# Kernel optimization log

Measured on AMD Instinct MI355X. Metric: run time of the kernel, lower is better.

## Reference

```python
import jax, jax.numpy as jnp
import numpy as np

D = 1024
H = 16
DH = D // H
L = 128  # max_pos_len
B = 4
T = 1024
SCALE = float(np.sqrt(D / H))


def setup_inputs() -> dict:
    key = jax.random.key(0)
    ks = jax.random.split(key, 9)
    x_q = jax.random.normal(ks[0], (B, T, D), dtype=jnp.float32)
    x_k = jax.random.normal(ks[1], (B, T, D), dtype=jnp.float32)
    x_v = jax.random.normal(ks[2], (B, T, D), dtype=jnp.float32)
    mask = jax.random.randint(ks[3], (B, 1, 1, T), 0, 2) == 1  # bool, True = masked
    Wq = jax.random.normal(ks[4], (D, D), dtype=jnp.float32) * 0.02
    Wk = jax.random.normal(ks[5], (D, D), dtype=jnp.float32) * 0.02
    Wv = jax.random.normal(ks[6], (D, D), dtype=jnp.float32) * 0.02
    Wo = jax.random.normal(ks[7], (D, D), dtype=jnp.float32) * 0.02
    pos_emb = jax.random.normal(ks[8], (2 * L + 1, DH), dtype=jnp.float32)
    return {"x_q": x_q, "x_k": x_k, "x_v": x_v, "mask": mask,
            "Wq": Wq, "Wk": Wk, "Wv": Wv, "Wo": Wo, "pos_emb": pos_emb}


def reference(x_q, x_k, x_v, mask, Wq, Wk, Wv, Wo, pos_emb):
    # nn.Linear(bias=False): y = x @ W.T
    def split_heads(x):  # (B,T,D) -> (B,H,T,DH)
        return x.reshape(B, -1, H, DH).transpose(0, 2, 1, 3)

    Q = split_heads(x_q @ Wq.T)
    K = split_heads(x_k @ Wk.T)
    V = split_heads(x_v @ Wv.T)

    logits = jnp.einsum('bhqd,bhkd->bhqk', Q, K)

    # arrange_char_pos_embedding: indices[q,k] = clamp(k-q, -L, L) + L
    rel = jnp.clip(jnp.arange(T)[None, :] - jnp.arange(T)[:, None], -L, L) + L
    arranged_pos = pos_emb[rel]  # (T_Q, T_K, DH)
    pos_logits = jnp.einsum('bhqd,qkd->bhqk', Q, arranged_pos)

    logits = (logits + pos_logits) / SCALE
    logits = jnp.where(mask, -jnp.inf, logits)  # mask broadcasts (B,1,1,T)
    attn = jax.nn.softmax(logits, axis=-1)  # dropout p=0.0 -> identity

    combined = jnp.einsum('bhqk,bhkd->bhqd', attn, V)
    heads_concat = combined.transpose(0, 2, 1, 3).reshape(B, -1, D)
    return heads_concat @ Wo.T
```

## Files before the change

kernel.cpp:

```cpp
#include <hip/hip_runtime.h>
#include <hip/hip_bf16.h>
#include <stdint.h>

typedef __attribute__((ext_vector_type(8))) short short8;
typedef __attribute__((ext_vector_type(4))) float f32x4;

__device__ __forceinline__ uint16_t f2bf(float f) {
    union { float f; uint32_t u; } v; v.f = f;
    uint32_t r = v.u + 0x7FFF + ((v.u >> 16) & 1);
    return (uint16_t)(r >> 16);
}
__device__ __forceinline__ float bf2f(uint16_t u) {
    union { uint32_t u; float f; } v; v.u = ((uint32_t)u) << 16;
    return v.f;
}
__device__ __forceinline__ float exp2_raw(float x) {
    float r;
    asm("v_exp_f32 %0, %1" : "=v"(r) : "v"(x));
    return r;
}
__device__ __forceinline__ uint32_t cvt_pk_bf16(float lo, float hi) {
    uint32_t r;
    asm("v_cvt_pk_bf16_f32 %0, %1, %2" : "=v"(r) : "v"(lo), "v"(hi));
    return r;
}

template<int F32>
__device__ __forceinline__ uint4 load8(const void* p, size_t off) {
    if (F32) {
        const float* f = (const float*)p + off;
        float4 f0 = *(const float4*)f;
        float4 f1 = *(const float4*)(f + 4);
        uint4 r;
        r.x = (uint32_t)f2bf(f0.x) | ((uint32_t)f2bf(f0.y) << 16);
        r.y = (uint32_t)f2bf(f0.z) | ((uint32_t)f2bf(f0.w) << 16);
        r.z = (uint32_t)f2bf(f1.x) | ((uint32_t)f2bf(f1.y) << 16);
        r.w = (uint32_t)f2bf(f1.z) | ((uint32_t)f2bf(f1.w) << 16);
        return r;
    } else {
        return *(const uint4*)((const uint16_t*)p + off);
    }
}

#define GLDS(gp, lp) __builtin_amdgcn_global_load_lds( \
    (const __attribute__((address_space(1))) void*)(gp), \
    (__attribute__((address_space(3))) void*)(lp), 16, 0, 0)

struct CvtSeg { const float* s; uint16_t* d; int n8; };
struct CvtArgs {
    CvtSeg seg[9]; int nseg;
    const void* mraw; unsigned long long* mbits; uint16_t* mvals;
};

__global__ __launch_bounds__(256) void cvt_bf16(CvtArgs a)
{
    if (blockIdx.x == 0) {
        __shared__ int flags[3];
        __shared__ uint8_t mloc[4096];
        const uint32_t* w = (const uint32_t*)a.mraw;
        const uint8_t* b8 = (const uint8_t*)a.mraw;
        const int t = threadIdx.x;
        if (t < 3) flags[t] = 0;
        __syncthreads();
        int fbyte = 0, ff32 = 0, fodd = 0;
        for (int i = t; i < 1024; i += 256) {
            uint32_t v = w[i];
            if (v != 0u && v != 1u && v != 0x3F800000u) fbyte = 1;
            if (v == 0x3F800000u) ff32 = 1;
            if ((i & 1) && v != 0u) fodd = 1;
        }
        if (fbyte) atomicOr(&flags[0], 1);
        if (ff32)  atomicOr(&flags[1], 1);
        if (fodd)  atomicOr(&flags[2], 1);
        __syncthreads();
        int mode;
        if (flags[0]) mode = 1;
        else if (flags[1]) mode = 0;
        else if (!flags[2]) mode = 2;
        else mode = 0;
        for (int k = t; k < 4096; k += 256) {
            int val;
            if (mode == 1)      val = (b8[k] != 0);
            else if (mode == 2) val = (w[2 * k] != 0u);
            else                val = (w[k] != 0u);
            mloc[k] = (uint8_t)val;
        }
        __syncthreads();
        for (int k = t; k < 4096; k += 256)
            a.mvals[k] = mloc[k] ? (uint16_t)0 : (uint16_t)0x3F80;
        if (t < 64) {
            uint64_t bits = 0;
#pragma unroll
            for (int i = 0; i < 64; ++i)
                bits |= (uint64_t)mloc[t * 64 + i] << i;
            a.mbits[t] = bits;
        }
    }
    const int tid = blockIdx.x * 256 + threadIdx.x;
    const int stride = gridDim.x * 256;
    for (int s = 0; s < a.nseg; ++s) {
        const float* src = a.seg[s].s;
        uint16_t* dst = a.seg[s].d;
        const int n8 = a.seg[s].n8;
        if (src) {
            for (int i = tid; i < n8; i += stride)
                *(uint4*)(dst + (size_t)i * 8) = load8<1>(src, (size_t)i * 8);
        } else {
            const uint4 z = {0u, 0u, 0u, 0u};
            for (int i = tid; i < n8; i += stride)
                *(uint4*)(dst + (size_t)i * 8) = z;
        }
    }
}

__global__ __launch_bounds__(256) void gemm128_qkv(
    const uint16_t* __restrict__ xq, const uint16_t* __restrict__ xk, const uint16_t* __restrict__ xv,
    const uint16_t* __restrict__ Wq, const uint16_t* __restrict__ Wk, const uint16_t* __restrict__ Wv,
    uint16_t* __restrict__ Qh, uint16_t* __restrict__ Khd, uint16_t* __restrict__ Vt,
    const unsigned long long* __restrict__ mbits)
{
    __shared__ alignas(16) uint16_t As[2][128 * 32];
    __shared__ alignas(16) uint16_t Bs[2][128 * 32];

    const int z = blockIdx.z;
    const uint16_t* A = (z == 0) ? xq : (z == 1) ? xk : xv;
    const uint16_t* B = (z == 0) ? Wq : (z == 1) ? Wk : Wv;
    uint16_t* C = (z == 0) ? Qh : (z == 1) ? Khd : Vt;
    const int cm = (z == 2) ? 2 : 1;
    const int bm = blockIdx.x, bn = blockIdx.y;
    const int K = 1024;

    const int t = threadIdx.x;
    const int lane = t & 63, wave = t >> 6;
    const int lrow = lane & 15, quad = lane >> 4;
    const int wr = (wave >> 1) * 64, wc = (wave & 1) * 64;
    const int g_row = wave * 16 + (lane >> 2);
    const int g_col = (lane & 3) * 8;

    const f32x4 fz = {0.f, 0.f, 0.f, 0.f};
    f32x4 acc[4][4];
#pragma unroll
    for (int i = 0; i < 4; ++i)
#pragma unroll
        for (int j = 0; j < 4; ++j) acc[i][j] = fz;

    for (int k0 = 0; k0 < K; k0 += 64) {
        __syncthreads();
#pragma unroll
        for (int kh = 0; kh < 2; ++kh) {
            const int kk = k0 + kh * 32;
            GLDS(A + (size_t)(bm * 128 + g_row) * K + kk + g_col,      As[kh] + wave * 512);
            GLDS(A + (size_t)(bm * 128 + g_row + 64) * K + kk + g_col, As[kh] + wave * 512 + 2048);
            GLDS(B + (size_t)(bn * 128 + g_row) * K + kk + g_col,      Bs[kh] + wave * 512);
            GLDS(B + (size_t)(bn * 128 + g_row + 64) * K + kk + g_col, Bs[kh] + wave * 512 + 2048);
        }
        __syncthreads();

#pragma unroll
        for (int kh = 0; kh < 2; ++kh) {
            short8 a[4], b[4];
#pragma unroll
            for (int i = 0; i < 4; ++i)
                a[i] = *(const short8*)(As[kh] + (wr + i * 16 + lrow) * 32 + quad * 8);
#pragma unroll
            for (int j = 0; j < 4; ++j)
                b[j] = *(const short8*)(Bs[kh] + (wc + j * 16 + lrow) * 32 + quad * 8);
#pragma unroll
            for (int i = 0; i < 4; ++i)
#pragma unroll
                for (int j = 0; j < 4; ++j)
                    acc[i][j] = __builtin_amdgcn_mfma_f32_16x16x32_bf16(a[i], b[j], acc[i][j], 0, 0, 0);
        }
    }

    if (cm == 2) {
        __syncthreads();
        uint16_t* scr = As[0] + wave * 1024;
        const int mg0 = bm * 128 + wr;
        const int widx = __builtin_amdgcn_readfirstlane((mg0 >> 10) * 16 + ((mg0 & 1023) >> 6));
        const uint64_t mword = mbits[widx];
        const uint64_t mw64 = mword >> ((lane & 1) * 8);
#pragma unroll
        for (int i = 0; i < 4; ++i)
#pragma unroll
            for (int j = 0; j < 4; ++j) {
                uint2 pk;
                pk.x = (uint32_t)f2bf(acc[i][j][0]) | ((uint32_t)f2bf(acc[i][j][1]) << 16);
                pk.y = (uint32_t)f2bf(acc[i][j][2]) | ((uint32_t)f2bf(acc[i][j][3]) << 16);
                *(uint2*)(scr + lrow * 16 + quad * 4) = pk;
                if (lane < 32) {
                    int n = lane >> 1, m8 = (lane & 1) * 8;
                    short8 vv = *(const short8*)(scr + n * 16 + m8);
                    int ng = bn * 128 + wc + j * 16 + n;
                    int hh = ng >> 6, d = ng & 63;
                    int mg = bm * 128 + wr + i * 16;
                    int bb = mg >> 10, tl = (mg & 1023) + m8;
                    uint32_t eb = (uint32_t)(mw64 >> (i * 16)) & 0xFFu;
                    if (eb) {
                        union { short8 s; uint32_t u[4]; } uw;
                        uw.s = vv;
#pragma unroll
                        for (int c = 0; c < 4; ++c) {
                            uint32_t km = (((eb >> (2 * c)) & 1) ? 0u : 0x0000FFFFu)
                                        | (((eb >> (2 * c + 1)) & 1) ? 0u : 0xFFFF0000u);
                            uw.u[c] &= km;
                        }
                        vv = uw.s;
                    }
                    size_t addr = (size_t)(bb * 16 + hh) * 65536
                                + (size_t)((tl >> 6) * 4096
                                           + ((d >> 4) * 2 + ((tl >> 5) & 1)) * 512
                                           + ((tl >> 3) & 3) * 128 + (d & 15) * 8);
                    *(short8*)(C + addr) = vv;
                }
            }
        return;
    }

#pragma unroll
    for (int i = 0; i < 4; ++i)
#pragma unroll
        for (int j = 0; j < 4; ++j)
#pragma unroll
            for (int r = 0; r < 4; ++r) {
                int m = bm * 128 + wr + i * 16 + quad * 4 + r;
                int n = bn * 128 + wc + j * 16 + lrow;
                int bb = m >> 10, tt = m & 1023, hh = n >> 6, d = n & 63;
                C[(((size_t)bb * 16 + hh) * 1024 + tt) * 64 + d] = f2bf(acc[i][j][r]);
            }
}

__global__ __launch_bounds__(256) void gemm_out(
    const uint16_t* __restrict__ A, const uint16_t* __restrict__ B,
    float* __restrict__ C, int M, int N, int K)
{
    __shared__ alignas(16) uint16_t As[2][64 * 32];
    __shared__ alignas(16) uint16_t Bs[2][128 * 32];

    const int t = threadIdx.x;
    const int lane = t & 63, wave = t >> 6;
    const int lrow = lane & 15, quad = lane >> 4;
    const int wr = (wave >> 1) * 32, wc = (wave & 1) * 64;
    const int g_row = wave * 16 + (lane >> 2);
    const int g_col = (lane & 3) * 8;
    const int bm = blockIdx.x, bn = blockIdx.y;

    const f32x4 fz = {0.f, 0.f, 0.f, 0.f};
    f32x4 acc[2][4];
#pragma unroll
    for (int i = 0; i < 2; ++i)
#pragma unroll
        for (int j = 0; j < 4; ++j) acc[i][j] = fz;

    for (int k0 = 0; k0 < K; k0 += 64) {
        __syncthreads();
#pragma unroll
        for (int kh = 0; kh < 2; ++kh) {
            const int kk = k0 + kh * 32;
            GLDS(A + (size_t)(bm * 64 + g_row) * K + kk + g_col,       As[kh] + wave * 512);
            GLDS(B + (size_t)(bn * 128 + g_row) * K + kk + g_col,      Bs[kh] + wave * 512);
            GLDS(B + (size_t)(bn * 128 + g_row + 64) * K + kk + g_col, Bs[kh] + wave * 512 + 2048);
        }
        __syncthreads();

#pragma unroll
        for (int kh = 0; kh < 2; ++kh) {
            short8 a[2], b[4];
#pragma unroll
            for (int i = 0; i < 2; ++i)
                a[i] = *(const short8*)(As[kh] + (wr + i * 16 + lrow) * 32 + quad * 8);
#pragma unroll
            for (int j = 0; j < 4; ++j)
                b[j] = *(const short8*)(Bs[kh] + (wc + j * 16 + lrow) * 32 + quad * 8);
#pragma unroll
            for (int i = 0; i < 2; ++i)
#pragma unroll
                for (int j = 0; j < 4; ++j)
                    acc[i][j] = __builtin_amdgcn_mfma_f32_16x16x32_bf16(a[i], b[j], acc[i][j], 0, 0, 0);
        }
    }

#pragma unroll
    for (int i = 0; i < 2; ++i)
#pragma unroll
        for (int j = 0; j < 4; ++j)
#pragma unroll
            for (int r = 0; r < 4; ++r) {
                int m = bm * 64 + wr + i * 16 + quad * 4 + r;
                int n = bn * 128 + wc + j * 16 + lrow;
                C[(size_t)m * N + n] = acc[i][j][r];
            }
}

#define FA_SM(KB_)                                                              \
{                                                                               \
    const int diff = (KB_) - qb;                                                \
    if (diff <= -192 || diff >= 144) {                                          \
        const bool low = (diff <= -192);                                        \
        _Pragma("unroll")                                                       \
        for (int j = 0; j < 4; ++j) {                                           \
            float e[4];                                                         \
            _Pragma("unroll")                                                   \
            for (int r = 0; r < 4; ++r) {                                       \
                float pc = low ? pcl[r] : pch[r];                               \
                e[r] = exp2_raw(__builtin_fmaf(s[j][r], CS, pc));               \
            }                                                                   \
            const uint32_t p01 = cvt_pk_bf16(e[0], e[1]);                       \
            const uint32_t p23 = cvt_pk_bf16(e[2], e[3]);                       \
            const int col = j * 16 + lrow;                                      \
            const int rw = quad * 4;                                            \
            Pl[wave][rw + 0][col] = (uint16_t)p01;                              \
            Pl[wave][rw + 1][col] = (uint16_t)(p01 >> 16);                      \
            Pl[wave][rw + 2][col] = (uint16_t)p23;                              \
            Pl[wave][rw + 3][col] = (uint16_t)(p23 >> 16);                      \
        }                                                                       \
    } else {                                                                    \
        _Pragma("unroll")                                                       \
        for (int j = 0; j < 4; ++j) {                                           \
            const int key = (KB_) + j * 16 + lrow;                              \
            float e[4];                                                         \
            _Pragma("unroll")                                                   \
            for (int r = 0; r < 4; ++r) {                                       \
                int q = qb + quad * 4 + r;                                      \
                int ql = q & 63;                                                \
                int rel = min(max(key - q, -128), 128) + 128;                   \
                float p = bf2f(Qpos_l[ql][rel]);                                \
                e[r] = exp2_raw(__builtin_fmaf(s[j][r], CS, p));                \
            }                                                                   \
            const uint32_t p01 = cvt_pk_bf16(e[0], e[1]);                       \
            const uint32_t p23 = cvt_pk_bf16(e[2], e[3]);                       \
            const int col = j * 16 + lrow;                                      \
            const int rw = quad * 4;                                            \
            Pl[wave][rw + 0][col] = (uint16_t)p01;                              \
            Pl[wave][rw + 1][col] = (uint16_t)(p01 >> 16);                      \
            Pl[wave][rw + 2][col] = (uint16_t)p23;                              \
            Pl[wave][rw + 3][col] = (uint16_t)(p23 >> 16);                      \
        }                                                                       \
    }                                                                           \
    ap0 = *(const short8*)(&Pl[wave][lrow][quad * 8]);                          \
    ap1 = *(const short8*)(&Pl[wave][lrow][32 + quad * 8]);                     \
}

__global__ __launch_bounds__(256, 3) void flash_attn(
    const uint16_t* __restrict__ Qh, const uint16_t* __restrict__ Kh,
    const uint16_t* __restrict__ Vt, const uint16_t* __restrict__ pos,
    const uint16_t* __restrict__ maskv, uint16_t* __restrict__ comb)
{
    const int blk = blockIdx.x;
    const int jj = blk >> 3;
    const int bh = (blk & 7) * 8 + (jj >> 4);
    const int qt = jj & 15;
    const int b = bh >> 4;
    const int h = bh & 15;
    const int t = threadIdx.x;
    const int lane = t & 63;
    const int wave = t >> 6;
    const int lrow = lane & 15;
    const int quad = lane >> 4;
    const int qb = qt * 64 + wave * 16;
    const int lane8 = lane * 8;

    __shared__ alignas(16) uint16_t Ks[4096];
    __shared__ alignas(16) uint16_t Qpos_l[64][277];
    __shared__ alignas(16) uint16_t Pl[4][16][72];

    const uint16_t* Kp = Kh + (size_t)bh * 65536;
    const uint16_t* Vp = Vt + (size_t)bh * 65536;
    const uint16_t* mkb = maskv + (size_t)b * 1024;

    const int sg_r = lane >> 2;
    const int sg_c = ((lane & 3) ^ ((sg_r >> 1) & 3)) * 8;
    const int hw = wave >> 1;
    const int gw = (wave & 1) * 2;
    const int rdc = (quad ^ ((lrow >> 1) & 3)) * 8;

    const float CS = 0.18033688011f;

#pragma unroll
    for (int gg = 0; gg < 2; ++gg) {
        int g = gw + gg;
        GLDS(Kp + (size_t)(g * 16 + sg_r) * 64 + hw * 32 + sg_c, &Ks[hw * 2048 + g * 512]);
    }

    const uint16_t* Qp = Qh + ((size_t)bh * 1024 + qb) * 64;
    short8 aq0 = *(const short8*)(Qp + (size_t)lrow * 64 + quad * 8);
    short8 aq1 = *(const short8*)(Qp + (size_t)lrow * 64 + 32 + quad * 8);

    const f32x4 fz = {0.f, 0.f, 0.f, 0.f};

#pragma unroll 4
    for (int nt = 0; nt < 17; ++nt) {
        short8 pb0 = *(const short8*)(pos + (size_t)(nt * 16 + lrow) * 64 + quad * 8);
        short8 pb1 = *(const short8*)(pos + (size_t)(nt * 16 + lrow) * 64 + 32 + quad * 8);
        f32x4 c = __builtin_amdgcn_mfma_f32_16x16x32_bf16(aq0, pb0, fz, 0, 0, 0);
        c = __builtin_amdgcn_mfma_f32_16x16x32_bf16(aq1, pb1, c, 0, 0, 0);
        const uint32_t p01 = cvt_pk_bf16(c[0] * CS, c[1] * CS);
        const uint32_t p23 = cvt_pk_bf16(c[2] * CS, c[3] * CS);
        const int row = wave * 16 + quad * 4;
        const int col = nt * 16 + lrow;
        Qpos_l[row + 0][col] = (uint16_t)p01;
        Qpos_l[row + 1][col] = (uint16_t)(p01 >> 16);
        Qpos_l[row + 2][col] = (uint16_t)p23;
        Qpos_l[row + 3][col] = (uint16_t)(p23 >> 16);
    }

    float pcl[4], pch[4];
#pragma unroll
    for (int r = 0; r < 4; ++r) {
        int ql = wave * 16 + quad * 4 + r;
        pcl[r] = bf2f(Qpos_l[ql][0]);
        pch[r] = bf2f(Qpos_l[ql][256]);
    }

    f32x4 o[4] = {fz, fz, fz, fz};
    f32x4 lacc = fz;
    short8 ap0, ap1;

    for (int ti = 0; ti < 16; ++ti) {
        const int kb = ti * 64;
        __syncthreads();
        short8 kr[8];
#pragma unroll
        for (int j = 0; j < 4; ++j) {
            kr[j * 2 + 0] = *(const short8*)(Ks + (j * 16 + lrow) * 32 + rdc);
            kr[j * 2 + 1] = *(const short8*)(Ks + 2048 + (j * 16 + lrow) * 32 + rdc);
        }
        __syncthreads();
        if (ti < 15) {
#pragma unroll
            for (int gg = 0; gg < 2; ++gg) {
                int g = gw + gg;
                GLDS(Kp + (size_t)(kb + 64 + g * 16 + sg_r) * 64 + hw * 32 + sg_c,
                     &Ks[hw * 2048 + g * 512]);
            }
        }
        const uint16_t* vb = Vp + (size_t)ti * 4096;
        short8 vv[8];
#pragma unroll
        for (int sl = 0; sl < 8; ++sl)
            vv[sl] = *(const short8*)(vb + sl * 512 + lane8);
        short8 bm0 = *(const short8*)(mkb + kb + quad * 8);
        short8 bm1 = *(const short8*)(mkb + kb + 32 + quad * 8);

        f32x4 s[4];
        __builtin_amdgcn_s_setprio(1);
#pragma unroll
        for (int j = 0; j < 4; ++j) {
            s[j] = __builtin_amdgcn_mfma_f32_16x16x32_bf16(aq0, kr[j * 2 + 0], fz, 0, 0, 0);
            s[j] = __builtin_amdgcn_mfma_f32_16x16x32_bf16(aq1, kr[j * 2 + 1], s[j], 0, 0, 0);
        }
        __builtin_amdgcn_s_setprio(0);

        FA_SM(kb)

        __builtin_amdgcn_s_setprio(1);
#pragma unroll
        for (int dt = 0; dt < 4; ++dt) {
            o[dt] = __builtin_amdgcn_mfma_f32_16x16x32_bf16(ap0, vv[dt * 2 + 0], o[dt], 0, 0, 0);
            o[dt] = __builtin_amdgcn_mfma_f32_16x16x32_bf16(ap1, vv[dt * 2 + 1], o[dt], 0, 0, 0);
        }
        lacc = __builtin_amdgcn_mfma_f32_16x16x32_bf16(ap0, bm0, lacc, 0, 0, 0);
        lacc = __builtin_amdgcn_mfma_f32_16x16x32_bf16(ap1, bm1, lacc, 0, 0, 0);
        __builtin_amdgcn_s_setprio(0);
    }

    float inv[4];
#pragma unroll
    for (int r = 0; r < 4; ++r) inv[r] = 1.0f / lacc[r];

#pragma unroll
    for (int dt = 0; dt < 4; ++dt)
#pragma unroll
        for (int r = 0; r < 4; ++r) {
            size_t row = (size_t)b * 1024 + qb + quad * 4 + r;
            size_t col = (size_t)h * 64 + dt * 16 + lrow;
            comb[row * 1024 + col] = f2bf(o[dt][r] * inv[r]);
        }
}

extern "C" void kernel_launch(void* const* d_in, const int* in_sizes, int n_in,
                              void* d_out, int out_size, void* d_ws, size_t ws_size,
                              hipStream_t stream)
{
    const float* x_q = (const float*)d_in[0];
    const float* x_k = (const float*)d_in[1];
    const float* x_v = (const float*)d_in[2];
    const void*  msk = d_in[3];
    const float* Wq  = (const float*)d_in[4];
    const float* Wk  = (const float*)d_in[5];
    const float* Wv  = (const float*)d_in[6];
    const float* Wo  = (const float*)d_in[7];
    const float* pos = (const float*)d_in[8];

    char* ws = (char*)d_ws;
    const size_t MB = 1u << 20;
    uint16_t* Qh   = (uint16_t*)(ws);
    uint16_t* Khd  = (uint16_t*)(ws + 8 * MB);
    uint16_t* Vt   = (uint16_t*)(ws + 16 * MB);
    uint16_t* xqb  = (uint16_t*)(ws + 24 * MB);
    uint16_t* xkb  = (uint16_t*)(ws + 32 * MB);
    uint16_t* xvb  = (uint16_t*)(ws + 40 * MB);
    uint16_t* Wqb  = (uint16_t*)(ws + 48 * MB);
    uint16_t* Wkb  = (uint16_t*)(ws + 50 * MB);
    uint16_t* Wvb  = (uint16_t*)(ws + 52 * MB);
    uint16_t* Wob  = (uint16_t*)(ws + 54 * MB);
    uint16_t* posb = (uint16_t*)(ws + 56 * MB);
    unsigned long long* mbits = (unsigned long long*)(ws + 56 * MB + 65536);
    uint16_t* mvals = (uint16_t*)(ws + 56 * MB + 65536 + 4096);
    uint16_t* comb = xqb;

    CvtArgs ca{};
    int ns = 0;
    ca.seg[ns++] = {x_q, xqb, 524288};
    ca.seg[ns++] = {x_k, xkb, 524288};
    ca.seg[ns++] = {x_v, xvb, 524288};
    ca.seg[ns++] = {Wq, Wqb, 131072};
    ca.seg[ns++] = {Wk, Wkb, 131072};
    ca.seg[ns++] = {Wv, Wvb, 131072};
    ca.seg[ns++] = {Wo, Wob, 131072};
    ca.seg[ns++] = {pos, posb, 2056};
    ca.seg[ns++] = {nullptr, posb + 16448, 120};
    ca.nseg = ns;
    ca.mraw = msk;
    ca.mbits = mbits;
    ca.mvals = mvals;
    cvt_bf16<<<dim3(512), dim3(256), 0, stream>>>(ca);

    gemm128_qkv<<<dim3(32, 8, 3), dim3(256), 0, stream>>>(
        xqb, xkb, xvb, Wqb, Wkb, Wvb, Qh, Khd, Vt, mbits);

    flash_attn<<<dim3(1024), dim3(256), 0, stream>>>(Qh, Khd, Vt, posb, mvals, comb);

    gemm_out<<<dim3(64, 8), dim3(256), 0, stream>>>(
        comb, Wob, (float*)d_out, 4096, 1024, 1024);
}
```

Before: 224.1 us.

## Software-pipeline PV MFMA one tile behind QK and softmax in flash attention

Restructures the key-tile loop so the P·V and row-sum MFMAs for tile ti-1 are issued alongside the QK MFMAs for tile ti, with a peeled prologue and epilogue. V and mask loads for a tile are issued after its softmax and consumed one iteration later, giving the global loads more time to land. The intent is to overlap MFMA work with the exp/softmax VALU phase and hide V load latency. In exchange, the V registers stay live across iterations, which raises register pressure under the 3-blocks-per-CU launch bound.

Measured after the change: 230.4 us. 1.03x slower.

```diff
diff --git a/kernel.cpp b/kernel.cpp
--- a/kernel.cpp
+++ b/kernel.cpp
@@ -341,6 +341,27 @@
     ap1 = *(const short8*)(&Pl[wave][lrow][32 + quad * 8]);                     \
 }
 
+#define FA_LOADV(TI_)                                                           \
+{                                                                               \
+    const uint16_t* vb = Vp + (size_t)(TI_) * 4096;                             \
+    _Pragma("unroll")                                                           \
+    for (int sl = 0; sl < 8; ++sl)                                              \
+        vv[sl] = *(const short8*)(vb + sl * 512 + lane8);                       \
+    bmc0 = *(const short8*)(mkb + (TI_) * 64 + quad * 8);                       \
+    bmc1 = *(const short8*)(mkb + (TI_) * 64 + 32 + quad * 8);                  \
+}
+
+#define FA_PV                                                                   \
+{                                                                               \
+    _Pragma("unroll")                                                           \
+    for (int dt = 0; dt < 4; ++dt) {                                            \
+        o[dt] = __builtin_amdgcn_mfma_f32_16x16x32_bf16(ap0, vv[dt * 2 + 0], o[dt], 0, 0, 0); \
+        o[dt] = __builtin_amdgcn_mfma_f32_16x16x32_bf16(ap1, vv[dt * 2 + 1], o[dt], 0, 0, 0); \
+    }                                                                           \
+    lacc = __builtin_amdgcn_mfma_f32_16x16x32_bf16(ap0, bmc0, lacc, 0, 0, 0);   \
+    lacc = __builtin_amdgcn_mfma_f32_16x16x32_bf16(ap1, bmc1, lacc, 0, 0, 0);   \
+}
+
 __global__ __launch_bounds__(256, 3) void flash_attn(
     const uint16_t* __restrict__ Qh, const uint16_t* __restrict__ Kh,
     const uint16_t* __restrict__ Vt, const uint16_t* __restrict__ pos,
@@ -414,9 +435,36 @@
 
     f32x4 o[4] = {fz, fz, fz, fz};
     f32x4 lacc = fz;
-    short8 ap0, ap1;
-
-    for (int ti = 0; ti < 16; ++ti) {
+    f32x4 s[4];
+    short8 ap0, ap1, vv[8], bmc0, bmc1;
+
+    {
+        __syncthreads();
+        short8 kr[8];
+#pragma unroll
+        for (int j = 0; j < 4; ++j) {
+            kr[j * 2 + 0] = *(const short8*)(Ks + (j * 16 + lrow) * 32 + rdc);
+            kr[j * 2 + 1] = *(const short8*)(Ks + 2048 + (j * 16 + lrow) * 32 + rdc);
+        }
+        __syncthreads();
+#pragma unroll
+        for (int gg = 0; gg < 2; ++gg) {
+            int g = gw + gg;
+            GLDS(Kp + (size_t)(64 + g * 16 + sg_r) * 64 + hw * 32 + sg_c,
+                 &Ks[hw * 2048 + g * 512]);
+        }
+        __builtin_amdgcn_s_setprio(1);
+#pragma unroll
+        for (int j = 0; j < 4; ++j) {
+            s[j] = __builtin_amdgcn_mfma_f32_16x16x32_bf16(aq0, kr[j * 2 + 0], fz, 0, 0, 0);
+            s[j] = __builtin_amdgcn_mfma_f32_16x16x32_bf16(aq1, kr[j * 2 + 1], s[j], 0, 0, 0);
+        }
+        __builtin_amdgcn_s_setprio(0);
+        FA_SM(0)
+        FA_LOADV(0)
+    }
+
+    for (int ti = 1; ti < 16; ++ti) {
         const int kb = ti * 64;
         __syncthreads();
         short8 kr[8];
@@ -434,35 +482,20 @@
                      &Ks[hw * 2048 + g * 512]);
             }
         }
-        const uint16_t* vb = Vp + (size_t)ti * 4096;
-        short8 vv[8];
-#pragma unroll
-        for (int sl = 0; sl < 8; ++sl)
-            vv[sl] = *(const short8*)(vb + sl * 512 + lane8);
-        short8 bm0 = *(const short8*)(mkb + kb + quad * 8);
-        short8 bm1 = *(const short8*)(mkb + kb + 32 + quad * 8);
-
-        f32x4 s[4];
         __builtin_amdgcn_s_setprio(1);
+        FA_PV
 #pragma unroll
         for (int j = 0; j < 4; ++j) {
             s[j] = __builtin_amdgcn_mfma_f32_16x16x32_bf16(aq0, kr[j * 2 + 0], fz, 0, 0, 0);
             s[j] = __builtin_amdgcn_mfma_f32_16x16x32_bf16(aq1, kr[j * 2 + 1], s[j], 0, 0, 0);
         }
         __builtin_amdgcn_s_setprio(0);
-
         FA_SM(kb)
-
-        __builtin_amdgcn_s_setprio(1);
-#pragma unroll
-        for (int dt = 0; dt < 4; ++dt) {
-            o[dt] = __builtin_amdgcn_mfma_f32_16x16x32_bf16(ap0, vv[dt * 2 + 0], o[dt], 0, 0, 0);
-            o[dt] = __builtin_amdgcn_mfma_f32_16x16x32_bf16(ap1, vv[dt * 2 + 1], o[dt], 0, 0, 0);
-        }
-        lacc = __builtin_amdgcn_mfma_f32_16x16x32_bf16(ap0, bm0, lacc, 0, 0, 0);
-        lacc = __builtin_amdgcn_mfma_f32_16x16x32_bf16(ap1, bm1, lacc, 0, 0, 0);
-        __builtin_amdgcn_s_setprio(0);
-    }
+        FA_LOADV(ti)
+    }
+    __builtin_amdgcn_s_setprio(1);
+    FA_PV
+    __builtin_amdgcn_s_setprio(0);
 
     float inv[4];
 #pragma unroll
```

## Pre-swizzle weights into MFMA fragment layout and load B directly to registers

Applied to the files above, without the earlier changes.

The weight conversion kernel now writes Wq/Wk/Wv/Wo in a fragment-major bf16 layout, so each wave in the QKV and output GEMMs can load its B operands straight from global memory into registers with contiguous 16-byte per-lane reads. This removes the B tiles from LDS, cutting LDS traffic and footprint, and launch bounds now request 3 blocks per CU for higher occupancy. The cost is that B is no longer shared through LDS, so the two waves covering the same columns both fetch it from global/L2, and the global loads are issued synchronously before the barrier, adding register pressure.

After: 225.5 us. About the same (+0.6%).

```diff
diff --git a/kernel.cpp b/kernel.cpp
--- a/kernel.cpp
+++ b/kernel.cpp
@@ -46,7 +46,7 @@
     (const __attribute__((address_space(1))) void*)(gp), \
     (__attribute__((address_space(3))) void*)(lp), 16, 0, 0)
 
-struct CvtSeg { const float* s; uint16_t* d; int n8; };
+struct CvtSeg { const float* s; uint16_t* d; int n8; int frag; };
 struct CvtArgs {
     CvtSeg seg[9]; int nseg;
     const void* mraw; unsigned long long* mbits; uint16_t* mvals;
@@ -103,8 +103,18 @@
         uint16_t* dst = a.seg[s].d;
         const int n8 = a.seg[s].n8;
         if (src) {
-            for (int i = tid; i < n8; i += stride)
-                *(uint4*)(dst + (size_t)i * 8) = load8<1>(src, (size_t)i * 8);
+            if (a.seg[s].frag) {
+                for (int i = tid; i < n8; i += stride) {
+                    const int n = i >> 7, k8 = i & 127;
+                    const size_t doff = (size_t)(
+                        (((k8 >> 3) * 2 + ((k8 >> 2) & 1)) * 64 + (n >> 4)) * 512
+                        + (k8 & 3) * 128 + (n & 15) * 8);
+                    *(uint4*)(dst + doff) = load8<1>(src, (size_t)i * 8);
+                }
+            } else {
+                for (int i = tid; i < n8; i += stride)
+                    *(uint4*)(dst + (size_t)i * 8) = load8<1>(src, (size_t)i * 8);
+            }
         } else {
             const uint4 z = {0u, 0u, 0u, 0u};
             for (int i = tid; i < n8; i += stride)
@@ -113,14 +123,13 @@
     }
 }
 
-__global__ __launch_bounds__(256) void gemm128_qkv(
+__global__ __launch_bounds__(256, 3) void gemm128_qkv(
     const uint16_t* __restrict__ xq, const uint16_t* __restrict__ xk, const uint16_t* __restrict__ xv,
     const uint16_t* __restrict__ Wq, const uint16_t* __restrict__ Wk, const uint16_t* __restrict__ Wv,
     uint16_t* __restrict__ Qh, uint16_t* __restrict__ Khd, uint16_t* __restrict__ Vt,
     const unsigned long long* __restrict__ mbits)
 {
     __shared__ alignas(16) uint16_t As[2][128 * 32];
-    __shared__ alignas(16) uint16_t Bs[2][128 * 32];
 
     const int z = blockIdx.z;
     const uint16_t* A = (z == 0) ? xq : (z == 1) ? xk : xv;
@@ -136,6 +145,8 @@
     const int wr = (wave >> 1) * 64, wc = (wave & 1) * 64;
     const int g_row = wave * 16 + (lane >> 2);
     const int g_col = (lane & 3) * 8;
+    const int nt_b = bn * 8 + (wave & 1) * 4;
+    const int lane8 = lane * 8;
 
     const f32x4 fz = {0.f, 0.f, 0.f, 0.f};
     f32x4 acc[4][4];
@@ -151,25 +162,39 @@
             const int kk = k0 + kh * 32;
             GLDS(A + (size_t)(bm * 128 + g_row) * K + kk + g_col,      As[kh] + wave * 512);
             GLDS(A + (size_t)(bm * 128 + g_row + 64) * K + kk + g_col, As[kh] + wave * 512 + 2048);
-            GLDS(B + (size_t)(bn * 128 + g_row) * K + kk + g_col,      Bs[kh] + wave * 512);
-            GLDS(B + (size_t)(bn * 128 + g_row + 64) * K + kk + g_col, Bs[kh] + wave * 512 + 2048);
-        }
-        __syncthreads();
-
-#pragma unroll
-        for (int kh = 0; kh < 2; ++kh) {
-            short8 a[4], b[4];
+        }
+        short8 b0[4], b1[4];
+        {
+            const uint16_t* bb = B + (size_t)(k0 >> 6) * 65536;
+#pragma unroll
+            for (int j = 0; j < 4; ++j) {
+                b0[j] = *(const short8*)(bb + (size_t)(nt_b + j) * 512 + lane8);
+                b1[j] = *(const short8*)(bb + 32768 + (size_t)(nt_b + j) * 512 + lane8);
+            }
+        }
+        __syncthreads();
+
+        {
+            short8 a[4];
 #pragma unroll
             for (int i = 0; i < 4; ++i)
-                a[i] = *(const short8*)(As[kh] + (wr + i * 16 + lrow) * 32 + quad * 8);
-#pragma unroll
-            for (int j = 0; j < 4; ++j)
-                b[j] = *(const short8*)(Bs[kh] + (wc + j * 16 + lrow) * 32 + quad * 8);
+                a[i] = *(const short8*)(As[0] + (wr + i * 16 + lrow) * 32 + quad * 8);
 #pragma unroll
             for (int i = 0; i < 4; ++i)
 #pragma unroll
                 for (int j = 0; j < 4; ++j)
-                    acc[i][j] = __builtin_amdgcn_mfma_f32_16x16x32_bf16(a[i], b[j], acc[i][j], 0, 0, 0);
+                    acc[i][j] = __builtin_amdgcn_mfma_f32_16x16x32_bf16(a[i], b0[j], acc[i][j], 0, 0, 0);
+        }
+        {
+            short8 a[4];
+#pragma unroll
+            for (int i = 0; i < 4; ++i)
+                a[i] = *(const short8*)(As[1] + (wr + i * 16 + lrow) * 32 + quad * 8);
+#pragma unroll
+            for (int i = 0; i < 4; ++i)
+#pragma unroll
+                for (int j = 0; j < 4; ++j)
+                    acc[i][j] = __builtin_amdgcn_mfma_f32_16x16x32_bf16(a[i], b1[j], acc[i][j], 0, 0, 0);
         }
     }
 
@@ -230,12 +255,11 @@
             }
 }
 
-__global__ __launch_bounds__(256) void gemm_out(
+__global__ __launch_bounds__(256, 3) void gemm_out(
     const uint16_t* __restrict__ A, const uint16_t* __restrict__ B,
     float* __restrict__ C, int M, int N, int K)
 {
     __shared__ alignas(16) uint16_t As[2][64 * 32];
-    __shared__ alignas(16) uint16_t Bs[2][128 * 32];
 
     const int t = threadIdx.x;
     const int lane = t & 63, wave = t >> 6;
@@ -244,6 +268,8 @@
     const int g_row = wave * 16 + (lane >> 2);
     const int g_col = (lane & 3) * 8;
     const int bm = blockIdx.x, bn = blockIdx.y;
+    const int nt_b = bn * 8 + (wave & 1) * 4;
+    const int lane8 = lane * 8;
 
     const f32x4 fz = {0.f, 0.f, 0.f, 0.f};
     f32x4 acc[2][4];
@@ -257,26 +283,40 @@
 #pragma unroll
         for (int kh = 0; kh < 2; ++kh) {
             const int kk = k0 + kh * 32;
-            GLDS(A + (size_t)(bm * 64 + g_row) * K + kk + g_col,       As[kh] + wave * 512);
-            GLDS(B + (size_t)(bn * 128 + g_row) * K + kk + g_col,      Bs[kh] + wave * 512);
-            GLDS(B + (size_t)(bn * 128 + g_row + 64) * K + kk + g_col, Bs[kh] + wave * 512 + 2048);
-        }
-        __syncthreads();
-
-#pragma unroll
-        for (int kh = 0; kh < 2; ++kh) {
-            short8 a[2], b[4];
+            GLDS(A + (size_t)(bm * 64 + g_row) * K + kk + g_col, As[kh] + wave * 512);
+        }
+        short8 b0[4], b1[4];
+        {
+            const uint16_t* bb = B + (size_t)(k0 >> 6) * 65536;
+#pragma unroll
+            for (int j = 0; j < 4; ++j) {
+                b0[j] = *(const short8*)(bb + (size_t)(nt_b + j) * 512 + lane8);
+                b1[j] = *(const short8*)(bb + 32768 + (size_t)(nt_b + j) * 512 + lane8);
+            }
+        }
+        __syncthreads();
+
+        {
+            short8 a[2];
 #pragma unroll
             for (int i = 0; i < 2; ++i)
-                a[i] = *(const short8*)(As[kh] + (wr + i * 16 + lrow) * 32 + quad * 8);
-#pragma unroll
-            for (int j = 0; j < 4; ++j)
-                b[j] = *(const short8*)(Bs[kh] + (wc + j * 16 + lrow) * 32 + quad * 8);
+                a[i] = *(const short8*)(As[0] + (wr + i * 16 + lrow) * 32 + quad * 8);
 #pragma unroll
             for (int i = 0; i < 2; ++i)
 #pragma unroll
                 for (int j = 0; j < 4; ++j)
-                    acc[i][j] = __builtin_amdgcn_mfma_f32_16x16x32_bf16(a[i], b[j], acc[i][j], 0, 0, 0);
+                    acc[i][j] = __builtin_amdgcn_mfma_f32_16x16x32_bf16(a[i], b0[j], acc[i][j], 0, 0, 0);
+        }
+        {
+            short8 a[2];
+#pragma unroll
+            for (int i = 0; i < 2; ++i)
+                a[i] = *(const short8*)(As[1] + (wr + i * 16 + lrow) * 32 + quad * 8);
+#pragma unroll
+            for (int i = 0; i < 2; ++i)
+#pragma unroll
+                for (int j = 0; j < 4; ++j)
+                    acc[i][j] = __builtin_amdgcn_mfma_f32_16x16x32_bf16(a[i], b1[j], acc[i][j], 0, 0, 0);
         }
     }
 
@@ -511,15 +551,15 @@
 
     CvtArgs ca{};
     int ns = 0;
-    ca.seg[ns++] = {x_q, xqb, 524288};
-    ca.seg[ns++] = {x_k, xkb, 524288};
-    ca.seg[ns++] = {x_v, xvb, 524288};
-    ca.seg[ns++] = {Wq, Wqb, 131072};
-    ca.seg[ns++] = {Wk, Wkb, 131072};
-    ca.seg[ns++] = {Wv, Wvb, 131072};
-    ca.seg[ns++] = {Wo, Wob, 131072};
-    ca.seg[ns++] = {pos, posb, 2056};
-    ca.seg[ns++] = {nullptr, posb + 16448, 120};
+    ca.seg[ns++] = {x_q, xqb, 524288, 0};
+    ca.seg[ns++] = {x_k, xkb, 524288, 0};
+    ca.seg[ns++] = {x_v, xvb, 524288, 0};
+    ca.seg[ns++] = {Wq, Wqb, 131072, 1};
+    ca.seg[ns++] = {Wk, Wkb, 131072, 1};
+    ca.seg[ns++] = {Wv, Wvb, 131072, 1};
+    ca.seg[ns++] = {Wo, Wob, 131072, 1};
+    ca.seg[ns++] = {pos, posb, 2056, 0};
+    ca.seg[ns++] = {nullptr, posb + 16448, 120, 0};
     ca.nseg = ns;
     ca.mraw = msk;
     ca.mbits = mbits;
```
